# Performance work log

Hardware: AMD Instinct MI355X
Metric: run time of the kernel (lower is better)

## Reference

```python
import jax, jax.numpy as jnp
import numpy as np

N_NODES = 50000
N_COLORS = 256
D = 64
H = 128  # MLP hidden = 2*D
E_VV = 800000
E_VC = 400000


def _mlp_params(key, d_in, d_hid, d_out):
    k1, k2 = jax.random.split(key)
    s1 = 1.0 / np.sqrt(d_in)
    s2 = 1.0 / np.sqrt(d_hid)
    return (
        jax.random.uniform(k1, (d_in, d_hid), jnp.float32, -s1, s1),
        jnp.zeros((d_hid,), jnp.float32),
        jax.random.uniform(k2, (d_hid, d_out), jnp.float32, -s2, s2),
        jnp.zeros((d_out,), jnp.float32),
    )


def setup_inputs() -> dict:
    key = jax.random.key(0)
    ks = jax.random.split(key, 8)
    x_v = jax.random.normal(ks[0], (N_NODES, D), jnp.float32)
    x_c = jax.random.normal(ks[1], (N_COLORS, D), jnp.float32)
    src_vv = jax.random.randint(ks[2], (E_VV,), 0, N_NODES, jnp.int32)
    dst_vv = jax.random.randint(ks[3], (E_VV,), 0, N_NODES, jnp.int32)
    src_vc = jax.random.randint(ks[4], (E_VC,), 0, N_COLORS, jnp.int32)
    dst_vc = jax.random.randint(ks[5], (E_VC,), 0, N_NODES, jnp.int32)
    W1v, b1v, W2v, b2v = _mlp_params(ks[6], D, H, D)
    W1c, b1c, W2c, b2c = _mlp_params(ks[7], D, H, D)
    return {
        "x_v": x_v, "x_c": x_c,
        "W1v": W1v, "b1v": b1v, "W2v": W2v, "b2v": b2v,
        "W1c": W1c, "b1c": b1c, "W2c": W2c, "b2c": b2c,
        "src_vv": src_vv, "dst_vv": dst_vv,
        "src_vc": src_vc, "dst_vc": dst_vc,
    }


def reference(x_v, x_c, W1v, b1v, W2v, b2v, W1c, b1c, W2c, b2c,
              src_vv, dst_vv, src_vc, dst_vc):
    n = x_v.shape[0]
    # vertex->vertex messages: gather, MLP, scatter-sum
    mv = jax.nn.relu(x_v[src_vv] @ W1v + b1v) @ W2v + b2v  # [E_vv, D]
    agg_v = jax.ops.segment_sum(mv, dst_vv, num_segments=n)
    # color->vertex messages: gather color embeddings, MLP, scatter-sum
    mc = jax.nn.relu(x_c[src_vc] @ W1c + b1c) @ W2c + b2c  # [E_vc, D]
    agg_c = jax.ops.segment_sum(mc, dst_vc, num_segments=n)
    return jax.nn.relu(x_v + agg_v + agg_c)
```

## Files before the change

kernel.cpp:

```cpp
#include <hip/hip_runtime.h>

#define NN 50000
#define NC 256
#define DD 64
#define HH 128
#define EVV 800000
#define EVC 400000
#define NE 1200000
#define NB 196
#define BCAP 8192
#define MLPV_B 196
#define MLPC_B 1
#define MLP_B (MLPV_B + MLPC_B)
#define FILL_EPB 8192
#define FILL_B 147
#define SEPT 50
#define K1_B (SEPT * 7)
#define GAT_B (NB * 2)
#define VCAP 64
#define ZROW (NN + NC)
#define HROW 136

typedef __attribute__((ext_vector_type(8))) short bf16x8;
typedef __attribute__((ext_vector_type(4))) float f32x4;

__device__ __forceinline__ unsigned short f2bf(float x) {
  unsigned u = __float_as_uint(x);
  u = (u + 0x7fffu + ((u >> 16) & 1u)) >> 16;
  return (unsigned short)u;
}

union SMem {
  unsigned short hl[16][16 * HROW];
  struct {
    int cnt[NB];
    int off[NB];
    int gbase[NB];
    int sa[256];
    unsigned int stage[FILL_EPB];
  } f;
};

__global__ __launch_bounds__(256) void prep_kernel(
    const float* __restrict__ W1v, const float* __restrict__ W2v,
    const float* __restrict__ W1c, const float* __restrict__ W2c,
    unsigned short* __restrict__ wt, int* __restrict__ gcur,
    unsigned short* __restrict__ table) {
  const int tid = blockIdx.x * 256 + threadIdx.x;
  if (tid < NB) gcur[tid] = 0;
  if (tid < DD) table[(size_t)ZROW * DD + tid] = 0;
  const int sel = tid >> 13;
  const int t = tid & 8191;
  unsigned short* dst = wt + sel * 8192;
  if (sel == 0) {
    const int n = t >> 6, k = t & 63;
    dst[t] = f2bf(W1v[k * HH + n]);
  } else if (sel == 1) {
    const int n = t >> 7, k = t & 127;
    dst[t] = f2bf(W2v[k * DD + n]);
  } else if (sel == 2) {
    const int n = t >> 6, k = t & 63;
    dst[t] = f2bf(W1c[k * HH + n]);
  } else {
    const int n = t >> 7, k = t & 127;
    dst[t] = f2bf(W2c[k * DD + n]);
  }
}

__device__ __forceinline__ void mlp_mfma(
    const float* __restrict__ X, const unsigned short* __restrict__ W1t,
    const float* __restrict__ b1, const unsigned short* __restrict__ W2t,
    const float* __restrict__ b2, unsigned short* __restrict__ Y, int blk,
    int nrows, unsigned short* __restrict__ hl) {
  const int lane = threadIdx.x & 63;
  const int m = lane & 15;
  const int quad = lane >> 4;
  const int rowbase = blk * 256 + (threadIdx.x >> 6) * 16;

  bf16x8 a0, a1;
  {
    float4 xa = {0.f, 0.f, 0.f, 0.f}, xb = xa, xc = xa, xd = xa;
    const int row = rowbase + m;
    if (row < nrows) {
      const float* xp = X + (size_t)row * DD + quad * 8;
      xa = *(const float4*)(xp);
      xb = *(const float4*)(xp + 4);
      xc = *(const float4*)(xp + 32);
      xd = *(const float4*)(xp + 36);
    }
    a0[0] = (short)f2bf(xa.x); a0[1] = (short)f2bf(xa.y);
    a0[2] = (short)f2bf(xa.z); a0[3] = (short)f2bf(xa.w);
    a0[4] = (short)f2bf(xb.x); a0[5] = (short)f2bf(xb.y);
    a0[6] = (short)f2bf(xb.z); a0[7] = (short)f2bf(xb.w);
    a1[0] = (short)f2bf(xc.x); a1[1] = (short)f2bf(xc.y);
    a1[2] = (short)f2bf(xc.z); a1[3] = (short)f2bf(xc.w);
    a1[4] = (short)f2bf(xd.x); a1[5] = (short)f2bf(xd.y);
    a1[6] = (short)f2bf(xd.z); a1[7] = (short)f2bf(xd.w);
  }

#pragma unroll
  for (int nt = 0; nt < 8; ++nt) {
    const int n = nt * 16 + m;
    const float bv = b1[n];
    f32x4 acc = {bv, bv, bv, bv};
    const bf16x8 b0 = *(const bf16x8*)(W1t + n * 64 + quad * 8);
    const bf16x8 b1f = *(const bf16x8*)(W1t + n * 64 + 32 + quad * 8);
    acc = __builtin_amdgcn_mfma_f32_16x16x32_bf16(a0, b0, acc, 0, 0, 0);
    acc = __builtin_amdgcn_mfma_f32_16x16x32_bf16(a1, b1f, acc, 0, 0, 0);
#pragma unroll
    for (int r = 0; r < 4; ++r)
      hl[(quad * 4 + r) * HROW + n] = f2bf(fmaxf(acc[r], 0.f));
  }

  bf16x8 ha[4];
#pragma unroll
  for (int kc = 0; kc < 4; ++kc)
    ha[kc] = *(const bf16x8*)(hl + m * HROW + kc * 32 + quad * 8);

#pragma unroll
  for (int nt = 0; nt < 4; ++nt) {
    const int n = nt * 16 + m;
    const float bv = b2[n];
    f32x4 acc = {bv, bv, bv, bv};
#pragma unroll
    for (int kc = 0; kc < 4; ++kc) {
      const bf16x8 bw = *(const bf16x8*)(W2t + n * 128 + kc * 32 + quad * 8);
      acc = __builtin_amdgcn_mfma_f32_16x16x32_bf16(ha[kc], bw, acc, 0, 0, 0);
    }
#pragma unroll
    for (int r = 0; r < 4; ++r) {
      const int row = rowbase + quad * 4 + r;
      if (row < nrows) Y[(size_t)row * DD + n] = f2bf(acc[r]);
    }
  }
}

__device__ __forceinline__ void fill_block(
    const int* __restrict__ src_vv, const int* __restrict__ dst_vv,
    const int* __restrict__ src_vc, const int* __restrict__ dst_vc,
    int* __restrict__ gcur, unsigned int* __restrict__ records, int blk,
    SMem* sm) {
  const int t = threadIdx.x;
  const int base = blk * FILL_EPB;
  if (t < NB) sm->f.cnt[t] = 0;
  __syncthreads();

  unsigned int rec[8];
  int rk[8];
#pragma unroll
  for (int r = 0; r < 8; ++r) {
    const int e = base + r * 1024 + t;
    rk[r] = -1;
    if (e < NE) {
      int s, d;
      if (e < EVV) {
        s = src_vv[e];
        d = dst_vv[e];
      } else {
        s = NN + src_vc[e - EVV];
        d = dst_vc[e - EVV];
      }
      rec[r] = ((unsigned int)d << 16) | (unsigned int)s;
      rk[r] = atomicAdd(&sm->f.cnt[d >> 8], 1);
    }
  }
  __syncthreads();

  if (t < 64) {
    int carry = 0;
    for (int ch = 0; ch < 4; ++ch) {
      const int idx = ch * 64 + t;
      int v = (idx < NB) ? sm->f.cnt[idx] : 0;
#pragma unroll
      for (int o = 1; o < 64; o <<= 1) {
        const int u = __shfl_up(v, o, 64);
        if (t >= o) v += u;
      }
      const int inc = v + carry;
      if (idx < NB) sm->f.sa[idx] = inc;
      carry = __shfl(inc, 63, 64);
    }
  }
  __syncthreads();

  if (t < NB) {
    const int val = sm->f.cnt[t];
    sm->f.off[t] = sm->f.sa[t] - val;
    sm->f.gbase[t] = t * BCAP + ((val > 0) ? atomicAdd(&gcur[t], val) : 0);
  }
  __syncthreads();

#pragma unroll
  for (int r = 0; r < 8; ++r)
    if (rk[r] >= 0) sm->f.stage[sm->f.off[rec[r] >> 24] + rk[r]] = rec[r];
  __syncthreads();

  const int total = (NE - base < FILL_EPB) ? (NE - base) : FILL_EPB;
  for (int i = t; i < total; i += 1024) {
    const unsigned int u = sm->f.stage[i];
    const int b2 = u >> 24;
    records[sm->f.gbase[b2] + (i - sm->f.off[b2])] = u;
  }
}

__global__ __launch_bounds__(1024) void k1_kernel(
    const float* __restrict__ x_v, const float* __restrict__ x_c,
    const float* __restrict__ b1v, const float* __restrict__ b2v,
    const float* __restrict__ b1c, const float* __restrict__ b2c,
    const unsigned short* __restrict__ wt,
    const int* __restrict__ src_vv, const int* __restrict__ dst_vv,
    const int* __restrict__ src_vc, const int* __restrict__ dst_vc,
    unsigned short* __restrict__ table, int* __restrict__ gcur,
    unsigned int* __restrict__ records) {
  __shared__ SMem sm;
  const int q = blockIdx.x / 7;
  const int r = blockIdx.x % 7;
  if (r < 3) {
    const int fid = q * 3 + r;
    if (fid >= FILL_B) return;
    fill_block(src_vv, dst_vv, src_vc, dst_vc, gcur, records, fid, &sm);
  } else {
    const int mb = q * 4 + (r - 3);
    if (mb >= MLP_B) return;
    unsigned short* hl = sm.hl[threadIdx.x >> 6];
    if (mb < MLPV_B)
      mlp_mfma(x_v, wt, b1v, wt + 8192, b2v, table, mb, NN, hl);
    else
      mlp_mfma(x_c, wt + 16384, b1c, wt + 24576, b2c,
               table + (size_t)NN * DD, mb - MLPV_B, NC, hl);
  }
}

__device__ __forceinline__ void acc8(float* a, const uint4 t) {
  a[0] += __uint_as_float(t.x << 16);
  a[1] += __uint_as_float(t.x & 0xffff0000u);
  a[2] += __uint_as_float(t.y << 16);
  a[3] += __uint_as_float(t.y & 0xffff0000u);
  a[4] += __uint_as_float(t.z << 16);
  a[5] += __uint_as_float(t.z & 0xffff0000u);
  a[6] += __uint_as_float(t.w << 16);
  a[7] += __uint_as_float(t.w & 0xffff0000u);
}

__device__ __forceinline__ void place(unsigned int u, unsigned int hsel,
                                      int* c1, unsigned short* slots) {
  const unsigned int lv = (u >> 16) & 255u;
  if ((lv & 128u) == hsel) {
    const int lg = (int)(lv & 127u);
    const int pos = atomicAdd(&c1[lg], 1);
    if (pos < VCAP) slots[lg * VCAP + pos] = (unsigned short)(u & 0xffffu);
  }
}

__global__ __launch_bounds__(1024) void gather_kernel(
    const uint4* __restrict__ table4, const unsigned int* __restrict__ records,
    const int* __restrict__ gcur, const float4* __restrict__ xv4,
    float4* __restrict__ out4) {
  __shared__ int c1[128];
  __shared__ unsigned short slots[128 * VCAP];
  const int t = threadIdx.x;
  const int bucket = blockIdx.x >> 1;
  const unsigned int hsel = (blockIdx.x & 1) << 7;
  const int start = bucket * BCAP;
  const int nrec = gcur[bucket];
  const int g = t >> 3;
  const int c = t & 7;
  const int v = bucket * 256 + (int)hsel + g;
  const size_t ob = (size_t)v * 16 + c * 2;

  float4 x0 = {0.f, 0.f, 0.f, 0.f}, x1 = x0;
  if (v < NN) {
    x0 = xv4[ob];
    x1 = xv4[ob + 1];
  }

  if (t < 128) c1[t] = 0;
  __syncthreads();

  const uint4* rec4 = (const uint4*)(records + start);
  const int nfull = nrec >> 2;
  for (int q = t; q < nfull; q += 1024) {
    const uint4 u = rec4[q];
    place(u.x, hsel, c1, slots);
    place(u.y, hsel, c1, slots);
    place(u.z, hsel, c1, slots);
    place(u.w, hsel, c1, slots);
  }
  for (int j = (nfull << 2) + t; j < nrec; j += 1024)
    place(records[start + j], hsel, c1, slots);
  __syncthreads();

  if (t < 128) {
    int n = c1[t];
    n = (n > VCAP) ? VCAP : n;
    const int np = (n + 7) & ~7;
    for (int i = n; i < np; ++i) slots[t * VCAP + i] = (unsigned short)ZROW;
    c1[t] = np;
  }
  __syncthreads();

  if (v >= NN) return;
  const int n = c1[g];
  const unsigned short* sl = slots + g * VCAP;

  float a[8];
#pragma unroll
  for (int r = 0; r < 8; ++r) a[r] = 0.f;

  for (int i = 0; i < n; i += 8) {
    const int e0 = sl[i + 0];
    const int e1 = sl[i + 1];
    const int e2 = sl[i + 2];
    const int e3 = sl[i + 3];
    const int e4 = sl[i + 4];
    const int e5 = sl[i + 5];
    const int e6 = sl[i + 6];
    const int e7 = sl[i + 7];
    const uint4 t0 = table4[(size_t)e0 * 8 + c];
    const uint4 t1 = table4[(size_t)e1 * 8 + c];
    const uint4 t2 = table4[(size_t)e2 * 8 + c];
    const uint4 t3 = table4[(size_t)e3 * 8 + c];
    const uint4 t4 = table4[(size_t)e4 * 8 + c];
    const uint4 t5 = table4[(size_t)e5 * 8 + c];
    const uint4 t6 = table4[(size_t)e6 * 8 + c];
    const uint4 t7 = table4[(size_t)e7 * 8 + c];
    acc8(a, t0); acc8(a, t1); acc8(a, t2); acc8(a, t3);
    acc8(a, t4); acc8(a, t5); acc8(a, t6); acc8(a, t7);
  }

  float4 o0, o1;
  o0.x = fmaxf(x0.x + a[0], 0.f);
  o0.y = fmaxf(x0.y + a[1], 0.f);
  o0.z = fmaxf(x0.z + a[2], 0.f);
  o0.w = fmaxf(x0.w + a[3], 0.f);
  o1.x = fmaxf(x1.x + a[4], 0.f);
  o1.y = fmaxf(x1.y + a[5], 0.f);
  o1.z = fmaxf(x1.z + a[6], 0.f);
  o1.w = fmaxf(x1.w + a[7], 0.f);
  out4[ob] = o0;
  out4[ob + 1] = o1;
}

extern "C" void kernel_launch(void* const* d_in, const int* in_sizes, int n_in,
                              void* d_out, int out_size, void* d_ws,
                              size_t ws_size, hipStream_t stream) {
  const float* x_v = (const float*)d_in[0];
  const float* x_c = (const float*)d_in[1];
  const float* W1v = (const float*)d_in[2];
  const float* b1v = (const float*)d_in[3];
  const float* W2v = (const float*)d_in[4];
  const float* b2v = (const float*)d_in[5];
  const float* W1c = (const float*)d_in[6];
  const float* b1c = (const float*)d_in[7];
  const float* W2c = (const float*)d_in[8];
  const float* b2c = (const float*)d_in[9];
  const int* src_vv = (const int*)d_in[10];
  const int* dst_vv = (const int*)d_in[11];
  const int* src_vc = (const int*)d_in[12];
  const int* dst_vc = (const int*)d_in[13];
  float* out = (float*)d_out;

  char* p = (char*)d_ws;
  unsigned short* table = (unsigned short*)p;
  p += (size_t)(NN + NC + 1) * DD * sizeof(unsigned short);
  unsigned int* records = (unsigned int*)p;
  p += (size_t)NB * BCAP * sizeof(unsigned int);
  unsigned short* wt = (unsigned short*)p;
  p += (size_t)4 * 8192 * sizeof(unsigned short);
  int* gcur = (int*)p;

  prep_kernel<<<128, 256, 0, stream>>>(W1v, W2v, W1c, W2c, wt, gcur, table);

  k1_kernel<<<K1_B, 1024, 0, stream>>>(x_v, x_c, b1v, b2v, b1c, b2c, wt,
                                       src_vv, dst_vv, src_vc, dst_vc, table,
                                       gcur, records);

  gather_kernel<<<GAT_B, 1024, 0, stream>>>((const uint4*)table, records, gcur,
                                            (const float4*)x_v, (float4*)out);
}
```

Baseline: 138.0 us.

## Split fused fill/MLP kernel into separate fill and small-block MLP kernels

The combined k1 kernel, which interleaved edge-bucketing fill blocks and MLP blocks inside 1024-thread workgroups sharing a union of LDS, is replaced by two kernels. The fill kernel runs 147 blocks of 1024 threads. The MLP kernel now runs 786 blocks of 256 threads, each handling 64 rows, so each block uses far less LDS and more workgroups fit per CU. The cost is an extra launch and serialization of the two phases, which previously overlapped within one launch.

```diff
diff --git a/kernel.cpp b/kernel.cpp
--- a/kernel.cpp
+++ b/kernel.cpp
@@ -9,13 +9,11 @@
 #define NE 1200000
 #define NB 196
 #define BCAP 8192
-#define MLPV_B 196
-#define MLPC_B 1
+#define MLPV_B 782
+#define MLPC_B 4
 #define MLP_B (MLPV_B + MLPC_B)
 #define FILL_EPB 8192
 #define FILL_B 147
-#define SEPT 50
-#define K1_B (SEPT * 7)
 #define GAT_B (NB * 2)
 #define VCAP 64
 #define ZROW (NN + NC)
@@ -29,17 +27,6 @@
   u = (u + 0x7fffu + ((u >> 16) & 1u)) >> 16;
   return (unsigned short)u;
 }
-
-union SMem {
-  unsigned short hl[16][16 * HROW];
-  struct {
-    int cnt[NB];
-    int off[NB];
-    int gbase[NB];
-    int sa[256];
-    unsigned int stage[FILL_EPB];
-  } f;
-};
 
 __global__ __launch_bounds__(256) void prep_kernel(
     const float* __restrict__ W1v, const float* __restrict__ W2v,
@@ -75,7 +62,7 @@
   const int lane = threadIdx.x & 63;
   const int m = lane & 15;
   const int quad = lane >> 4;
-  const int rowbase = blk * 256 + (threadIdx.x >> 6) * 16;
+  const int rowbase = blk * 64 + (threadIdx.x >> 6) * 16;
 
   bf16x8 a0, a1;
   {
@@ -135,14 +122,35 @@
   }
 }
 
-__device__ __forceinline__ void fill_block(
+__global__ __launch_bounds__(256) void mlp_kernel(
+    const float* __restrict__ x_v, const float* __restrict__ x_c,
+    const float* __restrict__ b1v, const float* __restrict__ b2v,
+    const float* __restrict__ b1c, const float* __restrict__ b2c,
+    const unsigned short* __restrict__ wt, unsigned short* __restrict__ table) {
+  __shared__ unsigned short hl4[4][16 * HROW];
+  const int mb = blockIdx.x;
+  unsigned short* hl = hl4[threadIdx.x >> 6];
+  if (mb < MLPV_B)
+    mlp_mfma(x_v, wt, b1v, wt + 8192, b2v, table, mb, NN, hl);
+  else
+    mlp_mfma(x_c, wt + 16384, b1c, wt + 24576, b2c,
+             table + (size_t)NN * DD, mb - MLPV_B, NC, hl);
+}
+
+__global__ __launch_bounds__(1024) void fill_kernel(
     const int* __restrict__ src_vv, const int* __restrict__ dst_vv,
     const int* __restrict__ src_vc, const int* __restrict__ dst_vc,
-    int* __restrict__ gcur, unsigned int* __restrict__ records, int blk,
-    SMem* sm) {
+    int* __restrict__ gcur, unsigned int* __restrict__ records) {
+  __shared__ struct {
+    int cnt[NB];
+    int off[NB];
+    int gbase[NB];
+    int sa[256];
+    unsigned int stage[FILL_EPB];
+  } f;
   const int t = threadIdx.x;
-  const int base = blk * FILL_EPB;
-  if (t < NB) sm->f.cnt[t] = 0;
+  const int base = blockIdx.x * FILL_EPB;
+  if (t < NB) f.cnt[t] = 0;
   __syncthreads();
 
   unsigned int rec[8];
@@ -161,7 +169,7 @@
         d = dst_vc[e - EVV];
       }
       rec[r] = ((unsigned int)d << 16) | (unsigned int)s;
-      rk[r] = atomicAdd(&sm->f.cnt[d >> 8], 1);
+      rk[r] = atomicAdd(&f.cnt[d >> 8], 1);
     }
   }
   __syncthreads();
@@ -170,64 +178,36 @@
     int carry = 0;
     for (int ch = 0; ch < 4; ++ch) {
       const int idx = ch * 64 + t;
-      int v = (idx < NB) ? sm->f.cnt[idx] : 0;
+      int v = (idx < NB) ? f.cnt[idx] : 0;
 #pragma unroll
       for (int o = 1; o < 64; o <<= 1) {
         const int u = __shfl_up(v, o, 64);
         if (t >= o) v += u;
       }
       const int inc = v + carry;
-      if (idx < NB) sm->f.sa[idx] = inc;
+      if (idx < NB) f.sa[idx] = inc;
       carry = __shfl(inc, 63, 64);
     }
   }
   __syncthreads();
 
   if (t < NB) {
-    const int val = sm->f.cnt[t];
-    sm->f.off[t] = sm->f.sa[t] - val;
-    sm->f.gbase[t] = t * BCAP + ((val > 0) ? atomicAdd(&gcur[t], val) : 0);
+    const int val = f.cnt[t];
+    f.off[t] = f.sa[t] - val;
+    f.gbase[t] = t * BCAP + ((val > 0) ? atomicAdd(&gcur[t], val) : 0);
   }
   __syncthreads();
 
 #pragma unroll
   for (int r = 0; r < 8; ++r)
-    if (rk[r] >= 0) sm->f.stage[sm->f.off[rec[r] >> 24] + rk[r]] = rec[r];
+    if (rk[r] >= 0) f.stage[f.off[rec[r] >> 24] + rk[r]] = rec[r];
   __syncthreads();
 
   const int total = (NE - base < FILL_EPB) ? (NE - base) : FILL_EPB;
   for (int i = t; i < total; i += 1024) {
-    const unsigned int u = sm->f.stage[i];
+    const unsigned int u = f.stage[i];
     const int b2 = u >> 24;
-    records[sm->f.gbase[b2] + (i - sm->f.off[b2])] = u;
-  }
-}
-
-__global__ __launch_bounds__(1024) void k1_kernel(
-    const float* __restrict__ x_v, const float* __restrict__ x_c,
-    const float* __restrict__ b1v, const float* __restrict__ b2v,
-    const float* __restrict__ b1c, const float* __restrict__ b2c,
-    const unsigned short* __restrict__ wt,
-    const int* __restrict__ src_vv, const int* __restrict__ dst_vv,
-    const int* __restrict__ src_vc, const int* __restrict__ dst_vc,
-    unsigned short* __restrict__ table, int* __restrict__ gcur,
-    unsigned int* __restrict__ records) {
-  __shared__ SMem sm;
-  const int q = blockIdx.x / 7;
-  const int r = blockIdx.x % 7;
-  if (r < 3) {
-    const int fid = q * 3 + r;
-    if (fid >= FILL_B) return;
-    fill_block(src_vv, dst_vv, src_vc, dst_vc, gcur, records, fid, &sm);
-  } else {
-    const int mb = q * 4 + (r - 3);
-    if (mb >= MLP_B) return;
-    unsigned short* hl = sm.hl[threadIdx.x >> 6];
-    if (mb < MLPV_B)
-      mlp_mfma(x_v, wt, b1v, wt + 8192, b2v, table, mb, NN, hl);
-    else
-      mlp_mfma(x_c, wt + 16384, b1c, wt + 24576, b2c,
-               table + (size_t)NN * DD, mb - MLPV_B, NC, hl);
+    records[f.gbase[b2] + (i - f.off[b2])] = u;
   }
 }
 
@@ -371,9 +351,11 @@
 
   prep_kernel<<<128, 256, 0, stream>>>(W1v, W2v, W1c, W2c, wt, gcur, table);
 
-  k1_kernel<<<K1_B, 1024, 0, stream>>>(x_v, x_c, b1v, b2v, b1c, b2c, wt,
-                                       src_vv, dst_vv, src_vc, dst_vc, table,
-                                       gcur, records);
+  fill_kernel<<<FILL_B, 1024, 0, stream>>>(src_vv, dst_vv, src_vc, dst_vc,
+                                           gcur, records);
+
+  mlp_kernel<<<MLP_B, 256, 0, stream>>>(x_v, x_c, b1v, b2v, b1c, b2c, wt,
+                                        table);
 
   gather_kernel<<<GAT_B, 1024, 0, stream>>>((const uint4*)table, records, gcur,
                                             (const float4*)x_v, (float4*)out);
```

New measurement: 142.4 us. +3.2%, slower.
